# Optimization experiments

Measured on AMD Instinct MI355X. Metric: run time of the kernel, lower is better.

## Reference

```python
import jax, jax.numpy as jnp
import numpy as np

B, S, D, H = 4, 2048, 1024, 16
DK = D // H  # 64


def setup_inputs() -> dict:
    key = jax.random.key(0)
    ks = jax.random.split(key, 5)
    scale = 1.0 / np.sqrt(D)
    return {
        "embeddings": jax.random.normal(ks[0], (B, S, D), dtype=jnp.float32),
        "W_q": jax.random.normal(ks[1], (D, D), dtype=jnp.float32) * scale,
        "W_k": jax.random.normal(ks[2], (D, D), dtype=jnp.float32) * scale,
        "W_v": jax.random.normal(ks[3], (D, D), dtype=jnp.float32) * scale,
        "W_o": jax.random.normal(ks[4], (D, D), dtype=jnp.float32) * scale,
    }


def reference(embeddings, W_q, W_k, W_v, W_o):
    # torch nn.Linear: y = x @ W.T  (weights are [out, in])
    b, s, d = embeddings.shape
    h, dk = H, DK
    q = embeddings @ W_q.T  # [b, s, d]
    k = embeddings @ W_k.T
    v = embeddings @ W_v.T
    # split heads along last dim (matches the per-head slicing in the torch loop)
    q = q.reshape(b, s, h, dk)
    k = k.reshape(b, s, h, dk)
    v = v.reshape(b, s, h, dk)
    scores = jnp.einsum("bqhd,bkhd->bhqk", q, k) / jnp.sqrt(jnp.float32(dk))
    p = jax.nn.softmax(scores, axis=-1)  # dropout is identity at eval
    ctx = jnp.einsum("bhqk,bkhd->bqhd", p, v).reshape(b, s, d)
    return ctx @ W_o.T
```

## Files before the change

### kernel.cpp

```cpp
#include <hip/hip_runtime.h>
#include <hip/hip_bf16.h>

typedef unsigned short u16;
typedef __attribute__((ext_vector_type(8))) short bf16x8;
typedef __attribute__((ext_vector_type(4))) float f32x4;

#define AS1 __attribute__((address_space(1)))
#define AS3 __attribute__((address_space(3)))

constexpr int Bc = 4, Sc = 2048, Dc = 1024, Hc = 16, DKc = 64;
constexpr size_t EDc = (size_t)Bc * Sc * Dc;
constexpr size_t WDc = (size_t)Dc * Dc;

__device__ __forceinline__ void g2l16(const void* g, void* l) {
  __builtin_amdgcn_global_load_lds((const AS1 unsigned int*)g,
                                   (AS3 unsigned int*)l, 16, 0, 0);
}

__device__ __forceinline__ u16 f2b(float f) {
  union { float f; unsigned u; } x; x.f = f;
  unsigned r = x.u + 0x7fffu + ((x.u >> 16) & 1u);
  return (u16)(r >> 16);
}

#if __has_builtin(__builtin_amdgcn_cvt_pk_bf16_f32)
typedef __attribute__((ext_vector_type(2))) __bf16 hbf2;
__device__ __forceinline__ unsigned f2b_pk(float a, float b) {
  union { hbf2 v; unsigned u; } x;
  x.v = __builtin_amdgcn_cvt_pk_bf16_f32(a, b);
  return x.u;
}
#else
__device__ __forceinline__ unsigned f2b_pk(float a, float b) {
  return (unsigned)f2b(a) | ((unsigned)f2b(b) << 16);
}
#endif

__device__ __forceinline__ float fast_exp2(float x) {
#if __has_builtin(__builtin_amdgcn_exp2f)
  return __builtin_amdgcn_exp2f(x);
#else
  return exp2f(x);
#endif
}

__global__ __launch_bounds__(256)
void cvt_all(const float* __restrict__ e, const float* __restrict__ wq,
             const float* __restrict__ wk, const float* __restrict__ wv,
             const float* __restrict__ wo, u16* __restrict__ dst) {
  int bx = blockIdx.x;
  const float* src;
  size_t doff;
  int chunk;
  if (bx < 4096) {
    src = e; doff = 0; chunk = bx;
  } else {
    int t = bx - 4096;
    int w = t >> 9;
    chunk = t & 511;
    src = (w == 0) ? wq : (w == 1) ? wk : (w == 2) ? wv : wo;
    doff = EDc + (size_t)w * WDc;
  }
  size_t i = ((size_t)chunk * 256 + threadIdx.x) * 8;
  float4 a = *(const float4*)(src + i);
  float4 b = *(const float4*)(src + i + 4);
  bf16x8 o;
  o[0] = (short)f2b(a.x); o[1] = (short)f2b(a.y);
  o[2] = (short)f2b(a.z); o[3] = (short)f2b(a.w);
  o[4] = (short)f2b(b.x); o[5] = (short)f2b(b.y);
  o[6] = (short)f2b(b.z); o[7] = (short)f2b(b.w);
  *(bf16x8*)(dst + doff + i) = o;
}

__global__ __launch_bounds__(256, 2)
void gemm_qkv(const u16* __restrict__ X, const u16* __restrict__ Wq,
              const u16* __restrict__ Wk, const u16* __restrict__ Wv,
              u16* __restrict__ Qo, u16* __restrict__ Ko,
              u16* __restrict__ VTo) {
  constexpr int BM = 128, BK = 64, K = Dc, N = Dc;
  __shared__ u16 As[BM * BK];
  __shared__ u16 Bs[BM * BK];

  const int tid = threadIdx.x;
  const int wave = tid >> 6, lane = tid & 63;
  const int mr = lane & 15, quad = lane >> 4, mr7 = lane & 7;
  const int hwlin = blockIdx.y * 24 + blockIdx.x;
  const int swz = (hwlin & 7) * 192 + (hwlin >> 3);
  const int lx = swz % 24, ly = swz / 24;
  const int sect = lx >> 3;
  const int n0 = (lx & 7) * 128;
  const int m0 = ly * BM;
  const u16* W = (sect == 0) ? Wq : (sect == 1) ? Wk : Wv;
  const int wm = (wave >> 1) * 64, wn = (wave & 1) * 64;
  const int ldr = lane >> 3;
  const int ldc_sw = ((lane & 7) ^ (ldr & 7)) * 8;
  const bool vsec = (sect == 2);

  const f32x4 zero = {0.f, 0.f, 0.f, 0.f};
  f32x4 acc[4][4];
  #pragma unroll
  for (int i = 0; i < 4; i++)
    #pragma unroll
    for (int j = 0; j < 4; j++) acc[i][j] = zero;

  for (int k0 = 0; k0 < K; k0 += BK) {
    __syncthreads();
    #pragma unroll
    for (int i = 0; i < 4; i++) {
      int row = wave * 32 + i * 8;
      g2l16(X + (size_t)(m0 + row + ldr) * K + k0 + ldc_sw, As + row * BK);
      g2l16(W + (size_t)(n0 + row + ldr) * K + k0 + ldc_sw, Bs + row * BK);
    }
    __syncthreads();

    #pragma unroll
    for (int c = 0; c < 2; c++) {
      bf16x8 a[4], b[4];
      #pragma unroll
      for (int i = 0; i < 4; i++)
        a[i] = *(const bf16x8*)(As + (wm + i * 16 + mr) * BK +
                                (((c * 4 + quad) ^ mr7) * 8));
      #pragma unroll
      for (int j = 0; j < 4; j++)
        b[j] = *(const bf16x8*)(Bs + (wn + j * 16 + mr) * BK +
                                (((c * 4 + quad) ^ mr7) * 8));
      if (vsec) {
        #pragma unroll
        for (int i = 0; i < 4; i++)
          #pragma unroll
          for (int j = 0; j < 4; j++)
            acc[i][j] = __builtin_amdgcn_mfma_f32_16x16x32_bf16(
                b[j], a[i], acc[i][j], 0, 0, 0);
      } else {
        #pragma unroll
        for (int i = 0; i < 4; i++)
          #pragma unroll
          for (int j = 0; j < 4; j++)
            acc[i][j] = __builtin_amdgcn_mfma_f32_16x16x32_bf16(
                a[i], b[j], acc[i][j], 0, 0, 0);
      }
    }
  }

  if (vsec) {
    #pragma unroll
    for (int i = 0; i < 4; i++) {
      int s_glob = m0 + wm + i * 16 + mr;
      int bb = s_glob >> 11, s = s_glob & 2047;
      int sp = (s & ~63) | (s & 32) | ((s & 12) << 1) | ((s & 16) >> 2) |
               (s & 3);
      #pragma unroll
      for (int j = 0; j < 4; j++) {
        int nbase = n0 + wn + j * 16 + quad * 4;
        #pragma unroll
        for (int r = 0; r < 4; r++) {
          int n = nbase + r;
          int h = n >> 6, d = n & 63;
          VTo[((size_t)((bb * Hc + h) * DKc + d)) * Sc + sp] = f2b(acc[i][j][r]);
        }
      }
    }
  } else {
    const float scale = (sect == 0) ? 0.18033688f : 1.0f;
    u16* Y = (sect == 0) ? Qo : Ko;
    #pragma unroll
    for (int i = 0; i < 4; i++)
      #pragma unroll
      for (int j = 0; j < 4; j++)
        #pragma unroll
        for (int r = 0; r < 4; r++) {
          int m = m0 + wm + i * 16 + quad * 4 + r;
          int n = n0 + wn + j * 16 + mr;
          Y[(size_t)m * N + n] = f2b(acc[i][j][r] * scale);
        }
  }
}

__global__ __launch_bounds__(256, 2)
void gemm_out(const u16* __restrict__ X, const u16* __restrict__ W,
              float* __restrict__ Y, int M, int N, int K) {
  constexpr int BM = 128, BK = 64;
  __shared__ u16 As[BM * BK];
  __shared__ u16 Bs[BM * BK];

  const int tid = threadIdx.x;
  const int wave = tid >> 6, lane = tid & 63;
  const int mr = lane & 15, quad = lane >> 4, mr7 = lane & 7;
  const int hwlin = blockIdx.y * 8 + blockIdx.x;
  const int swz = (hwlin & 7) * 64 + (hwlin >> 3);
  const int m0 = (swz >> 3) * BM, n0 = (swz & 7) * BM;
  const int wm = (wave >> 1) * 64, wn = (wave & 1) * 64;
  const int ldr = lane >> 3;
  const int ldc_sw = ((lane & 7) ^ (ldr & 7)) * 8;

  const f32x4 zero = {0.f, 0.f, 0.f, 0.f};
  f32x4 acc[4][4];
  #pragma unroll
  for (int i = 0; i < 4; i++)
    #pragma unroll
    for (int j = 0; j < 4; j++) acc[i][j] = zero;

  for (int k0 = 0; k0 < K; k0 += BK) {
    __syncthreads();
    #pragma unroll
    for (int i = 0; i < 4; i++) {
      int row = wave * 32 + i * 8;
      g2l16(X + (size_t)(m0 + row + ldr) * K + k0 + ldc_sw, As + row * BK);
      g2l16(W + (size_t)(n0 + row + ldr) * K + k0 + ldc_sw, Bs + row * BK);
    }
    __syncthreads();

    #pragma unroll
    for (int c = 0; c < 2; c++) {
      bf16x8 a[4], b[4];
      #pragma unroll
      for (int i = 0; i < 4; i++)
        a[i] = *(const bf16x8*)(As + (wm + i * 16 + mr) * BK +
                                (((c * 4 + quad) ^ mr7) * 8));
      #pragma unroll
      for (int j = 0; j < 4; j++)
        b[j] = *(const bf16x8*)(Bs + (wn + j * 16 + mr) * BK +
                                (((c * 4 + quad) ^ mr7) * 8));
      #pragma unroll
      for (int i = 0; i < 4; i++)
        #pragma unroll
        for (int j = 0; j < 4; j++)
          acc[i][j] = __builtin_amdgcn_mfma_f32_16x16x32_bf16(
              a[i], b[j], acc[i][j], 0, 0, 0);
    }
  }

  #pragma unroll
  for (int i = 0; i < 4; i++)
    #pragma unroll
    for (int j = 0; j < 4; j++)
      #pragma unroll
      for (int r = 0; r < 4; r++) {
        int m = m0 + wm + i * 16 + quad * 4 + r;
        int n = n0 + wn + j * 16 + mr;
        Y[(size_t)m * N + n] = acc[i][j][r];
      }
}

__global__ __launch_bounds__(512, 4)
void attn(const u16* __restrict__ Q, const u16* __restrict__ K,
          const u16* __restrict__ VT, u16* __restrict__ O) {
  __shared__ u16 Ks[2][64 * 64];
  __shared__ u16 Vs[2][64 * 64];

  const int tid = threadIdx.x;
  const int wave = tid >> 6, lane = tid & 63;
  const int mr = lane & 15, quad = lane >> 4, mr7 = lane & 7;
  const int hwlin = blockIdx.y * 8 + blockIdx.x;
  const int swz = (hwlin & 7) * 64 + (hwlin >> 3);
  const int bh = swz >> 3;
  const int q0 = (swz & 7) * 256;
  const int b = bh >> 4, h = bh & 15;
  const size_t headK = (size_t)b * Sc * Dc + (size_t)h * DKc;
  const size_t headV = (size_t)bh * DKc * Sc;
  const int ldr = lane >> 3;
  const int ldc_sw = ((lane & 7) ^ (ldr & 7)) * 8;

  const int row0 = wave * 8;
  const int pr = row0 + ldr;

  bf16x8 qa[2][2];
  #pragma unroll
  for (int sub = 0; sub < 2; sub++)
    #pragma unroll
    for (int c = 0; c < 2; c++)
      qa[sub][c] = *(const bf16x8*)(Q + headK +
          (size_t)(q0 + wave * 32 + sub * 16 + mr) * Dc + c * 32 + quad * 8);

  const f32x4 zero = {0.f, 0.f, 0.f, 0.f};
  const short one_bf = (short)0x3F80;
  const bf16x8 ones = {one_bf, one_bf, one_bf, one_bf,
                       one_bf, one_bf, one_bf, one_bf};
  f32x4 o[2][4];
  f32x4 lacc[2];
  #pragma unroll
  for (int sub = 0; sub < 2; sub++) {
    lacc[sub] = zero;
    #pragma unroll
    for (int i = 0; i < 4; i++) o[sub][i] = zero;
  }

  g2l16(K + headK + (size_t)pr * Dc + ldc_sw, Ks[0] + row0 * 64);
  g2l16(VT + headV + (size_t)pr * Sc + ldc_sw, Vs[0] + row0 * 64);
  __syncthreads();

  union W8 { unsigned u[4]; bf16x8 v; };

  for (int kt = 0; kt < Sc / 64; kt++) {
    const int cur = kt & 1;
    if (kt + 1 < Sc / 64) {
      const int nk0 = (kt + 1) * 64;
      const int nxt = cur ^ 1;
      g2l16(K + headK + (size_t)(nk0 + pr) * Dc + ldc_sw, Ks[nxt] + row0 * 64);
      g2l16(VT + headV + (size_t)pr * Sc + nk0 + ldc_sw, Vs[nxt] + row0 * 64);
    }

    f32x4 s0[4], s1[4];
    #pragma unroll
    for (int kc = 0; kc < 4; kc++) {
      bf16x8 k0 = *(const bf16x8*)(Ks[cur] + (kc * 16 + mr) * 64 +
                                   ((quad ^ mr7) * 8));
      bf16x8 k1 = *(const bf16x8*)(Ks[cur] + (kc * 16 + mr) * 64 +
                                   (((4 + quad) ^ mr7) * 8));
      __builtin_amdgcn_s_setprio(1);
      s0[kc] = __builtin_amdgcn_mfma_f32_16x16x32_bf16(k0, qa[0][0], zero, 0, 0, 0);
      s1[kc] = __builtin_amdgcn_mfma_f32_16x16x32_bf16(k0, qa[1][0], zero, 0, 0, 0);
      s0[kc] = __builtin_amdgcn_mfma_f32_16x16x32_bf16(k1, qa[0][1], s0[kc], 0, 0, 0);
      s1[kc] = __builtin_amdgcn_mfma_f32_16x16x32_bf16(k1, qa[1][1], s1[kc], 0, 0, 0);
      __builtin_amdgcn_s_setprio(0);
    }

    W8 paw[2][2];
    {
      float e[16];
      #pragma unroll
      for (int kc = 0; kc < 4; kc++)
        #pragma unroll
        for (int r = 0; r < 4; r++)
          e[kc * 4 + r] = fast_exp2(s0[kc][r]);
      paw[0][0].u[0] = f2b_pk(e[0], e[1]);
      paw[0][0].u[1] = f2b_pk(e[2], e[3]);
      paw[0][0].u[2] = f2b_pk(e[4], e[5]);
      paw[0][0].u[3] = f2b_pk(e[6], e[7]);
      paw[0][1].u[0] = f2b_pk(e[8], e[9]);
      paw[0][1].u[1] = f2b_pk(e[10], e[11]);
      paw[0][1].u[2] = f2b_pk(e[12], e[13]);
      paw[0][1].u[3] = f2b_pk(e[14], e[15]);
    }
    {
      float e[16];
      #pragma unroll
      for (int kc = 0; kc < 4; kc++)
        #pragma unroll
        for (int r = 0; r < 4; r++)
          e[kc * 4 + r] = fast_exp2(s1[kc][r]);
      paw[1][0].u[0] = f2b_pk(e[0], e[1]);
      paw[1][0].u[1] = f2b_pk(e[2], e[3]);
      paw[1][0].u[2] = f2b_pk(e[4], e[5]);
      paw[1][0].u[3] = f2b_pk(e[6], e[7]);
      paw[1][1].u[0] = f2b_pk(e[8], e[9]);
      paw[1][1].u[1] = f2b_pk(e[10], e[11]);
      paw[1][1].u[2] = f2b_pk(e[12], e[13]);
      paw[1][1].u[3] = f2b_pk(e[14], e[15]);
    }

    __builtin_amdgcn_s_setprio(1);
    lacc[0] = __builtin_amdgcn_mfma_f32_16x16x32_bf16(
        paw[0][0].v, ones, lacc[0], 0, 0, 0);
    lacc[0] = __builtin_amdgcn_mfma_f32_16x16x32_bf16(
        paw[0][1].v, ones, lacc[0], 0, 0, 0);
    lacc[1] = __builtin_amdgcn_mfma_f32_16x16x32_bf16(
        paw[1][0].v, ones, lacc[1], 0, 0, 0);
    lacc[1] = __builtin_amdgcn_mfma_f32_16x16x32_bf16(
        paw[1][1].v, ones, lacc[1], 0, 0, 0);
    __builtin_amdgcn_s_setprio(0);

    #pragma unroll
    for (int ni = 0; ni < 4; ni++) {
      bf16x8 v0 = *(const bf16x8*)(Vs[cur] + (ni * 16 + mr) * 64 +
                                   ((quad ^ mr7) * 8));
      bf16x8 v1 = *(const bf16x8*)(Vs[cur] + (ni * 16 + mr) * 64 +
                                   (((4 + quad) ^ mr7) * 8));
      __builtin_amdgcn_s_setprio(1);
      o[0][ni] = __builtin_amdgcn_mfma_f32_16x16x32_bf16(
          paw[0][0].v, v0, o[0][ni], 0, 0, 0);
      o[1][ni] = __builtin_amdgcn_mfma_f32_16x16x32_bf16(
          paw[1][0].v, v0, o[1][ni], 0, 0, 0);
      o[0][ni] = __builtin_amdgcn_mfma_f32_16x16x32_bf16(
          paw[0][1].v, v1, o[0][ni], 0, 0, 0);
      o[1][ni] = __builtin_amdgcn_mfma_f32_16x16x32_bf16(
          paw[1][1].v, v1, o[1][ni], 0, 0, 0);
      __builtin_amdgcn_s_setprio(0);
    }

    __syncthreads();
  }

  #pragma unroll
  for (int sub = 0; sub < 2; sub++) {
    #pragma unroll
    for (int r = 0; r < 4; r++) {
      float inv = 1.0f / lacc[sub][r];
      int qq = q0 + wave * 32 + sub * 16 + quad * 4 + r;
      #pragma unroll
      for (int ni = 0; ni < 4; ni++)
        O[headK + (size_t)qq * Dc + ni * 16 + mr] = f2b(o[sub][ni][r] * inv);
    }
  }
}

extern "C" void kernel_launch(void* const* d_in, const int* in_sizes, int n_in,
                              void* d_out, int out_size, void* d_ws, size_t ws_size,
                              hipStream_t stream) {
  const float* emb = (const float*)d_in[0];
  const float* Wq  = (const float*)d_in[1];
  const float* Wk  = (const float*)d_in[2];
  const float* Wv  = (const float*)d_in[3];
  const float* Wo  = (const float*)d_in[4];
  float* out = (float*)d_out;

  const int M = Bc * Sc;

  u16* Eb  = (u16*)d_ws;
  u16* Wqb = Eb  + EDc;
  u16* Wkb = Wqb + WDc;
  u16* Wvb = Wkb + WDc;
  u16* Wob = Wvb + WDc;
  u16* Qb  = Wob + WDc;
  u16* Kb  = Qb  + EDc;
  u16* VTb = Kb  + EDc;
  u16* Cb  = Qb;

  dim3 blk(256);
  cvt_all<<<dim3(4096 + 4 * 512), blk, 0, stream>>>(emb, Wq, Wk, Wv, Wo, Eb);

  gemm_qkv<<<dim3(24, M / 128), blk, 0, stream>>>(Eb, Wqb, Wkb, Wvb,
                                                  Qb, Kb, VTb);

  attn<<<dim3(Sc / 256, Bc * Hc), dim3(512), 0, stream>>>(Qb, Kb, VTb, Cb);

  gemm_out<<<dim3(Dc / 128, M / 128), blk, 0, stream>>>(Cb, Wob, out,
                                                        M, Dc, Dc);
}
```

Before: 257.5 us.

## Software-pipeline attention: overlap QK^T of tile k with PV of tile k-1

Restructures the attention inner loop so each iteration computes scores and exponentials for the current KV tile while doing the row-sum and PV MFMAs for the previous tile's probabilities. V gets a triple-buffered LDS slot so the previous tile's values stay resident while the next one is prefetched. The loop is unrolled by two with ping-pong probability registers, and a drain step after the loop handles the last tile. The aim is to let exp/convert VALU work overlap with MFMA work, at the cost of more registers and LDS that could reduce occupancy.

```diff
diff --git a/kernel.cpp b/kernel.cpp
--- a/kernel.cpp
+++ b/kernel.cpp
@@ -246,7 +246,7 @@
 void attn(const u16* __restrict__ Q, const u16* __restrict__ K,
           const u16* __restrict__ VT, u16* __restrict__ O) {
   __shared__ u16 Ks[2][64 * 64];
-  __shared__ u16 Vs[2][64 * 64];
+  __shared__ u16 Vs[3][64 * 64];
 
   const int tid = threadIdx.x;
   const int wave = tid >> 6, lane = tid & 63;
@@ -285,101 +285,121 @@
     for (int i = 0; i < 4; i++) o[sub][i] = zero;
   }
 
+  union W8 { unsigned u[4]; bf16x8 v; };
+  W8 pawA[2][2], pawB[2][2];
+  #pragma unroll
+  for (int sb = 0; sb < 2; sb++)
+    #pragma unroll
+    for (int hh = 0; hh < 2; hh++) {
+      pawA[sb][hh].u[0] = 0; pawA[sb][hh].u[1] = 0;
+      pawA[sb][hh].u[2] = 0; pawA[sb][hh].u[3] = 0;
+    }
+
   g2l16(K + headK + (size_t)pr * Dc + ldc_sw, Ks[0] + row0 * 64);
   g2l16(VT + headV + (size_t)pr * Sc + ldc_sw, Vs[0] + row0 * 64);
   __syncthreads();
 
-  union W8 { unsigned u[4]; bf16x8 v; };
-
-  for (int kt = 0; kt < Sc / 64; kt++) {
-    const int cur = kt & 1;
+  int c0 = 0, cprev = 0;
+
+  auto body = [&](int kt, W8 (&pprev)[2][2], W8 (&pnew)[2][2]) {
+    const int curK = kt & 1;
+    const int cw = (c0 == 2) ? 0 : c0 + 1;
+    const int cp = cprev;
     if (kt + 1 < Sc / 64) {
       const int nk0 = (kt + 1) * 64;
-      const int nxt = cur ^ 1;
-      g2l16(K + headK + (size_t)(nk0 + pr) * Dc + ldc_sw, Ks[nxt] + row0 * 64);
-      g2l16(VT + headV + (size_t)pr * Sc + nk0 + ldc_sw, Vs[nxt] + row0 * 64);
-    }
-
-    f32x4 s0[4], s1[4];
-    #pragma unroll
-    for (int kc = 0; kc < 4; kc++) {
-      bf16x8 k0 = *(const bf16x8*)(Ks[cur] + (kc * 16 + mr) * 64 +
-                                   ((quad ^ mr7) * 8));
-      bf16x8 k1 = *(const bf16x8*)(Ks[cur] + (kc * 16 + mr) * 64 +
-                                   (((4 + quad) ^ mr7) * 8));
+      g2l16(K + headK + (size_t)(nk0 + pr) * Dc + ldc_sw,
+            Ks[curK ^ 1] + row0 * 64);
+      g2l16(VT + headV + (size_t)pr * Sc + nk0 + ldc_sw,
+            Vs[cw] + row0 * 64);
+    }
+
+    #pragma unroll
+    for (int sub = 0; sub < 2; sub++) {
+      f32x4 s[4];
       __builtin_amdgcn_s_setprio(1);
-      s0[kc] = __builtin_amdgcn_mfma_f32_16x16x32_bf16(k0, qa[0][0], zero, 0, 0, 0);
-      s1[kc] = __builtin_amdgcn_mfma_f32_16x16x32_bf16(k0, qa[1][0], zero, 0, 0, 0);
-      s0[kc] = __builtin_amdgcn_mfma_f32_16x16x32_bf16(k1, qa[0][1], s0[kc], 0, 0, 0);
-      s1[kc] = __builtin_amdgcn_mfma_f32_16x16x32_bf16(k1, qa[1][1], s1[kc], 0, 0, 0);
+      #pragma unroll
+      for (int kc = 0; kc < 4; kc++) {
+        bf16x8 k0 = *(const bf16x8*)(Ks[curK] + (kc * 16 + mr) * 64 +
+                                     ((quad ^ mr7) * 8));
+        bf16x8 k1 = *(const bf16x8*)(Ks[curK] + (kc * 16 + mr) * 64 +
+                                     (((4 + quad) ^ mr7) * 8));
+        s[kc] = __builtin_amdgcn_mfma_f32_16x16x32_bf16(
+            k0, qa[sub][0], zero, 0, 0, 0);
+        s[kc] = __builtin_amdgcn_mfma_f32_16x16x32_bf16(
+            k1, qa[sub][1], s[kc], 0, 0, 0);
+      }
       __builtin_amdgcn_s_setprio(0);
-    }
-
-    W8 paw[2][2];
-    {
-      float e[16];
-      #pragma unroll
-      for (int kc = 0; kc < 4; kc++)
-        #pragma unroll
-        for (int r = 0; r < 4; r++)
-          e[kc * 4 + r] = fast_exp2(s0[kc][r]);
-      paw[0][0].u[0] = f2b_pk(e[0], e[1]);
-      paw[0][0].u[1] = f2b_pk(e[2], e[3]);
-      paw[0][0].u[2] = f2b_pk(e[4], e[5]);
-      paw[0][0].u[3] = f2b_pk(e[6], e[7]);
-      paw[0][1].u[0] = f2b_pk(e[8], e[9]);
-      paw[0][1].u[1] = f2b_pk(e[10], e[11]);
-      paw[0][1].u[2] = f2b_pk(e[12], e[13]);
-      paw[0][1].u[3] = f2b_pk(e[14], e[15]);
-    }
-    {
-      float e[16];
-      #pragma unroll
-      for (int kc = 0; kc < 4; kc++)
-        #pragma unroll
-        for (int r = 0; r < 4; r++)
-          e[kc * 4 + r] = fast_exp2(s1[kc][r]);
-      paw[1][0].u[0] = f2b_pk(e[0], e[1]);
-      paw[1][0].u[1] = f2b_pk(e[2], e[3]);
-      paw[1][0].u[2] = f2b_pk(e[4], e[5]);
-      paw[1][0].u[3] = f2b_pk(e[6], e[7]);
-      paw[1][1].u[0] = f2b_pk(e[8], e[9]);
-      paw[1][1].u[1] = f2b_pk(e[10], e[11]);
-      paw[1][1].u[2] = f2b_pk(e[12], e[13]);
-      paw[1][1].u[3] = f2b_pk(e[14], e[15]);
+      pnew[sub][0].u[0] = f2b_pk(fast_exp2(s[0][0]), fast_exp2(s[0][1]));
+      pnew[sub][0].u[1] = f2b_pk(fast_exp2(s[0][2]), fast_exp2(s[0][3]));
+      pnew[sub][0].u[2] = f2b_pk(fast_exp2(s[1][0]), fast_exp2(s[1][1]));
+      pnew[sub][0].u[3] = f2b_pk(fast_exp2(s[1][2]), fast_exp2(s[1][3]));
+      pnew[sub][1].u[0] = f2b_pk(fast_exp2(s[2][0]), fast_exp2(s[2][1]));
+      pnew[sub][1].u[1] = f2b_pk(fast_exp2(s[2][2]), fast_exp2(s[2][3]));
+      pnew[sub][1].u[2] = f2b_pk(fast_exp2(s[3][0]), fast_exp2(s[3][1]));
+      pnew[sub][1].u[3] = f2b_pk(fast_exp2(s[3][2]), fast_exp2(s[3][3]));
     }
 
     __builtin_amdgcn_s_setprio(1);
     lacc[0] = __builtin_amdgcn_mfma_f32_16x16x32_bf16(
-        paw[0][0].v, ones, lacc[0], 0, 0, 0);
+        pprev[0][0].v, ones, lacc[0], 0, 0, 0);
     lacc[0] = __builtin_amdgcn_mfma_f32_16x16x32_bf16(
-        paw[0][1].v, ones, lacc[0], 0, 0, 0);
+        pprev[0][1].v, ones, lacc[0], 0, 0, 0);
     lacc[1] = __builtin_amdgcn_mfma_f32_16x16x32_bf16(
-        paw[1][0].v, ones, lacc[1], 0, 0, 0);
+        pprev[1][0].v, ones, lacc[1], 0, 0, 0);
     lacc[1] = __builtin_amdgcn_mfma_f32_16x16x32_bf16(
-        paw[1][1].v, ones, lacc[1], 0, 0, 0);
+        pprev[1][1].v, ones, lacc[1], 0, 0, 0);
+    #pragma unroll
+    for (int ni = 0; ni < 4; ni++) {
+      bf16x8 v0 = *(const bf16x8*)(Vs[cp] + (ni * 16 + mr) * 64 +
+                                   ((quad ^ mr7) * 8));
+      bf16x8 v1 = *(const bf16x8*)(Vs[cp] + (ni * 16 + mr) * 64 +
+                                   (((4 + quad) ^ mr7) * 8));
+      o[0][ni] = __builtin_amdgcn_mfma_f32_16x16x32_bf16(
+          pprev[0][0].v, v0, o[0][ni], 0, 0, 0);
+      o[1][ni] = __builtin_amdgcn_mfma_f32_16x16x32_bf16(
+          pprev[1][0].v, v0, o[1][ni], 0, 0, 0);
+      o[0][ni] = __builtin_amdgcn_mfma_f32_16x16x32_bf16(
+          pprev[0][1].v, v1, o[0][ni], 0, 0, 0);
+      o[1][ni] = __builtin_amdgcn_mfma_f32_16x16x32_bf16(
+          pprev[1][1].v, v1, o[1][ni], 0, 0, 0);
+    }
     __builtin_amdgcn_s_setprio(0);
 
-    #pragma unroll
-    for (int ni = 0; ni < 4; ni++) {
-      bf16x8 v0 = *(const bf16x8*)(Vs[cur] + (ni * 16 + mr) * 64 +
-                                   ((quad ^ mr7) * 8));
-      bf16x8 v1 = *(const bf16x8*)(Vs[cur] + (ni * 16 + mr) * 64 +
-                                   (((4 + quad) ^ mr7) * 8));
-      __builtin_amdgcn_s_setprio(1);
-      o[0][ni] = __builtin_amdgcn_mfma_f32_16x16x32_bf16(
-          paw[0][0].v, v0, o[0][ni], 0, 0, 0);
-      o[1][ni] = __builtin_amdgcn_mfma_f32_16x16x32_bf16(
-          paw[1][0].v, v0, o[1][ni], 0, 0, 0);
-      o[0][ni] = __builtin_amdgcn_mfma_f32_16x16x32_bf16(
-          paw[0][1].v, v1, o[0][ni], 0, 0, 0);
-      o[1][ni] = __builtin_amdgcn_mfma_f32_16x16x32_bf16(
-          paw[1][1].v, v1, o[1][ni], 0, 0, 0);
-      __builtin_amdgcn_s_setprio(0);
-    }
-
     __syncthreads();
-  }
+    cprev = c0;
+    c0 = cw;
+  };
+
+  for (int kt = 0; kt < Sc / 64; kt += 2) {
+    body(kt, pawA, pawB);
+    body(kt + 1, pawB, pawA);
+  }
+
+  __builtin_amdgcn_s_setprio(1);
+  lacc[0] = __builtin_amdgcn_mfma_f32_16x16x32_bf16(
+      pawA[0][0].v, ones, lacc[0], 0, 0, 0);
+  lacc[0] = __builtin_amdgcn_mfma_f32_16x16x32_bf16(
+      pawA[0][1].v, ones, lacc[0], 0, 0, 0);
+  lacc[1] = __builtin_amdgcn_mfma_f32_16x16x32_bf16(
+      pawA[1][0].v, ones, lacc[1], 0, 0, 0);
+  lacc[1] = __builtin_amdgcn_mfma_f32_16x16x32_bf16(
+      pawA[1][1].v, ones, lacc[1], 0, 0, 0);
+  #pragma unroll
+  for (int ni = 0; ni < 4; ni++) {
+    bf16x8 v0 = *(const bf16x8*)(Vs[cprev] + (ni * 16 + mr) * 64 +
+                                 ((quad ^ mr7) * 8));
+    bf16x8 v1 = *(const bf16x8*)(Vs[cprev] + (ni * 16 + mr) * 64 +
+                                 (((4 + quad) ^ mr7) * 8));
+    o[0][ni] = __builtin_amdgcn_mfma_f32_16x16x32_bf16(
+        pawA[0][0].v, v0, o[0][ni], 0, 0, 0);
+    o[1][ni] = __builtin_amdgcn_mfma_f32_16x16x32_bf16(
+        pawA[1][0].v, v0, o[1][ni], 0, 0, 0);
+    o[0][ni] = __builtin_amdgcn_mfma_f32_16x16x32_bf16(
+        pawA[0][1].v, v1, o[0][ni], 0, 0, 0);
+    o[1][ni] = __builtin_amdgcn_mfma_f32_16x16x32_bf16(
+        pawA[1][1].v, v1, o[1][ni], 0, 0, 0);
+  }
+  __builtin_amdgcn_s_setprio(0);
 
   #pragma unroll
   for (int sub = 0; sub < 2; sub++) {
```

Result: slower. 265.5 us (+3.1%).

## Halve attention query tile to 128 rows, doubling grid size

Applied to the files above, without the earlier changes.

Each attention block now handles 128 query rows (16 per wave) instead of 256 (32 per wave), and the grid doubles to 1024 blocks with the block-index swizzle adjusted to match. This cuts registers per thread and gives more blocks for filling CUs and hiding latency. In exchange, each K/V tile loaded into LDS is reused by half as many queries, so total K/V global traffic and LDS reads per unit of MFMA work double. The priority-raise region also now spans the PV MFMA loop as a whole.

```diff
diff --git a/kernel.cpp b/kernel.cpp
--- a/kernel.cpp
+++ b/kernel.cpp
@@ -251,10 +251,10 @@
   const int tid = threadIdx.x;
   const int wave = tid >> 6, lane = tid & 63;
   const int mr = lane & 15, quad = lane >> 4, mr7 = lane & 7;
-  const int hwlin = blockIdx.y * 8 + blockIdx.x;
-  const int swz = (hwlin & 7) * 64 + (hwlin >> 3);
-  const int bh = swz >> 3;
-  const int q0 = (swz & 7) * 256;
+  const int hwlin = blockIdx.y * 16 + blockIdx.x;
+  const int swz = (hwlin & 7) * 128 + (hwlin >> 3);
+  const int bh = swz >> 4;
+  const int q0 = (swz & 15) * 128;
   const int b = bh >> 4, h = bh & 15;
   const size_t headK = (size_t)b * Sc * Dc + (size_t)h * DKc;
   const size_t headV = (size_t)bh * DKc * Sc;
@@ -264,26 +264,20 @@
   const int row0 = wave * 8;
   const int pr = row0 + ldr;
 
-  bf16x8 qa[2][2];
-  #pragma unroll
-  for (int sub = 0; sub < 2; sub++)
-    #pragma unroll
-    for (int c = 0; c < 2; c++)
-      qa[sub][c] = *(const bf16x8*)(Q + headK +
-          (size_t)(q0 + wave * 32 + sub * 16 + mr) * Dc + c * 32 + quad * 8);
+  bf16x8 qa[2];
+  #pragma unroll
+  for (int c = 0; c < 2; c++)
+    qa[c] = *(const bf16x8*)(Q + headK +
+        (size_t)(q0 + wave * 16 + mr) * Dc + c * 32 + quad * 8);
 
   const f32x4 zero = {0.f, 0.f, 0.f, 0.f};
   const short one_bf = (short)0x3F80;
   const bf16x8 ones = {one_bf, one_bf, one_bf, one_bf,
                        one_bf, one_bf, one_bf, one_bf};
-  f32x4 o[2][4];
-  f32x4 lacc[2];
-  #pragma unroll
-  for (int sub = 0; sub < 2; sub++) {
-    lacc[sub] = zero;
-    #pragma unroll
-    for (int i = 0; i < 4; i++) o[sub][i] = zero;
-  }
+  f32x4 o[4];
+  f32x4 lacc = zero;
+  #pragma unroll
+  for (int i = 0; i < 4; i++) o[i] = zero;
 
   g2l16(K + headK + (size_t)pr * Dc + ldc_sw, Ks[0] + row0 * 64);
   g2l16(VT + headV + (size_t)pr * Sc + ldc_sw, Vs[0] + row0 * 64);
@@ -300,7 +294,7 @@
       g2l16(VT + headV + (size_t)pr * Sc + nk0 + ldc_sw, Vs[nxt] + row0 * 64);
     }
 
-    f32x4 s0[4], s1[4];
+    f32x4 s[4];
     #pragma unroll
     for (int kc = 0; kc < 4; kc++) {
       bf16x8 k0 = *(const bf16x8*)(Ks[cur] + (kc * 16 + mr) * 64 +
@@ -308,57 +302,24 @@
       bf16x8 k1 = *(const bf16x8*)(Ks[cur] + (kc * 16 + mr) * 64 +
                                    (((4 + quad) ^ mr7) * 8));
       __builtin_amdgcn_s_setprio(1);
-      s0[kc] = __builtin_amdgcn_mfma_f32_16x16x32_bf16(k0, qa[0][0], zero, 0, 0, 0);
-      s1[kc] = __builtin_amdgcn_mfma_f32_16x16x32_bf16(k0, qa[1][0], zero, 0, 0, 0);
-      s0[kc] = __builtin_amdgcn_mfma_f32_16x16x32_bf16(k1, qa[0][1], s0[kc], 0, 0, 0);
-      s1[kc] = __builtin_amdgcn_mfma_f32_16x16x32_bf16(k1, qa[1][1], s1[kc], 0, 0, 0);
+      s[kc] = __builtin_amdgcn_mfma_f32_16x16x32_bf16(k0, qa[0], zero, 0, 0, 0);
+      s[kc] = __builtin_amdgcn_mfma_f32_16x16x32_bf16(k1, qa[1], s[kc], 0, 0, 0);
       __builtin_amdgcn_s_setprio(0);
     }
 
-    W8 paw[2][2];
-    {
-      float e[16];
-      #pragma unroll
-      for (int kc = 0; kc < 4; kc++)
-        #pragma unroll
-        for (int r = 0; r < 4; r++)
-          e[kc * 4 + r] = fast_exp2(s0[kc][r]);
-      paw[0][0].u[0] = f2b_pk(e[0], e[1]);
-      paw[0][0].u[1] = f2b_pk(e[2], e[3]);
-      paw[0][0].u[2] = f2b_pk(e[4], e[5]);
-      paw[0][0].u[3] = f2b_pk(e[6], e[7]);
-      paw[0][1].u[0] = f2b_pk(e[8], e[9]);
-      paw[0][1].u[1] = f2b_pk(e[10], e[11]);
-      paw[0][1].u[2] = f2b_pk(e[12], e[13]);
-      paw[0][1].u[3] = f2b_pk(e[14], e[15]);
-    }
-    {
-      float e[16];
-      #pragma unroll
-      for (int kc = 0; kc < 4; kc++)
-        #pragma unroll
-        for (int r = 0; r < 4; r++)
-          e[kc * 4 + r] = fast_exp2(s1[kc][r]);
-      paw[1][0].u[0] = f2b_pk(e[0], e[1]);
-      paw[1][0].u[1] = f2b_pk(e[2], e[3]);
-      paw[1][0].u[2] = f2b_pk(e[4], e[5]);
-      paw[1][0].u[3] = f2b_pk(e[6], e[7]);
-      paw[1][1].u[0] = f2b_pk(e[8], e[9]);
-      paw[1][1].u[1] = f2b_pk(e[10], e[11]);
-      paw[1][1].u[2] = f2b_pk(e[12], e[13]);
-      paw[1][1].u[3] = f2b_pk(e[14], e[15]);
-    }
+    W8 paw0, paw1;
+    paw0.u[0] = f2b_pk(fast_exp2(s[0][0]), fast_exp2(s[0][1]));
+    paw0.u[1] = f2b_pk(fast_exp2(s[0][2]), fast_exp2(s[0][3]));
+    paw0.u[2] = f2b_pk(fast_exp2(s[1][0]), fast_exp2(s[1][1]));
+    paw0.u[3] = f2b_pk(fast_exp2(s[1][2]), fast_exp2(s[1][3]));
+    paw1.u[0] = f2b_pk(fast_exp2(s[2][0]), fast_exp2(s[2][1]));
+    paw1.u[1] = f2b_pk(fast_exp2(s[2][2]), fast_exp2(s[2][3]));
+    paw1.u[2] = f2b_pk(fast_exp2(s[3][0]), fast_exp2(s[3][1]));
+    paw1.u[3] = f2b_pk(fast_exp2(s[3][2]), fast_exp2(s[3][3]));
 
     __builtin_amdgcn_s_setprio(1);
-    lacc[0] = __builtin_amdgcn_mfma_f32_16x16x32_bf16(
-        paw[0][0].v, ones, lacc[0], 0, 0, 0);
-    lacc[0] = __builtin_amdgcn_mfma_f32_16x16x32_bf16(
-        paw[0][1].v, ones, lacc[0], 0, 0, 0);
-    lacc[1] = __builtin_amdgcn_mfma_f32_16x16x32_bf16(
-        paw[1][0].v, ones, lacc[1], 0, 0, 0);
-    lacc[1] = __builtin_amdgcn_mfma_f32_16x16x32_bf16(
-        paw[1][1].v, ones, lacc[1], 0, 0, 0);
-    __builtin_amdgcn_s_setprio(0);
+    lacc = __builtin_amdgcn_mfma_f32_16x16x32_bf16(paw0.v, ones, lacc, 0, 0, 0);
+    lacc = __builtin_amdgcn_mfma_f32_16x16x32_bf16(paw1.v, ones, lacc, 0, 0, 0);
 
     #pragma unroll
     for (int ni = 0; ni < 4; ni++) {
@@ -366,31 +327,21 @@
                                    ((quad ^ mr7) * 8));
       bf16x8 v1 = *(const bf16x8*)(Vs[cur] + (ni * 16 + mr) * 64 +
                                    (((4 + quad) ^ mr7) * 8));
-      __builtin_amdgcn_s_setprio(1);
-      o[0][ni] = __builtin_amdgcn_mfma_f32_16x16x32_bf16(
-          paw[0][0].v, v0, o[0][ni], 0, 0, 0);
-      o[1][ni] = __builtin_amdgcn_mfma_f32_16x16x32_bf16(
-          paw[1][0].v, v0, o[1][ni], 0, 0, 0);
-      o[0][ni] = __builtin_amdgcn_mfma_f32_16x16x32_bf16(
-          paw[0][1].v, v1, o[0][ni], 0, 0, 0);
-      o[1][ni] = __builtin_amdgcn_mfma_f32_16x16x32_bf16(
-          paw[1][1].v, v1, o[1][ni], 0, 0, 0);
-      __builtin_amdgcn_s_setprio(0);
-    }
-
-    __syncthreads();
-  }
-
-  #pragma unroll
-  for (int sub = 0; sub < 2; sub++) {
-    #pragma unroll
-    for (int r = 0; r < 4; r++) {
-      float inv = 1.0f / lacc[sub][r];
-      int qq = q0 + wave * 32 + sub * 16 + quad * 4 + r;
-      #pragma unroll
-      for (int ni = 0; ni < 4; ni++)
-        O[headK + (size_t)qq * Dc + ni * 16 + mr] = f2b(o[sub][ni][r] * inv);
-    }
+      o[ni] = __builtin_amdgcn_mfma_f32_16x16x32_bf16(paw0.v, v0, o[ni], 0, 0, 0);
+      o[ni] = __builtin_amdgcn_mfma_f32_16x16x32_bf16(paw1.v, v1, o[ni], 0, 0, 0);
+    }
+    __builtin_amdgcn_s_setprio(0);
+
+    __syncthreads();
+  }
+
+  #pragma unroll
+  for (int r = 0; r < 4; r++) {
+    float inv = 1.0f / lacc[r];
+    int qq = q0 + wave * 16 + quad * 4 + r;
+    #pragma unroll
+    for (int ni = 0; ni < 4; ni++)
+      O[headK + (size_t)qq * Dc + ni * 16 + mr] = f2b(o[ni][r] * inv);
   }
 }
 
@@ -422,7 +373,7 @@
   gemm_qkv<<<dim3(24, M / 128), blk, 0, stream>>>(Eb, Wqb, Wkb, Wvb,
                                                   Qb, Kb, VTb);
 
-  attn<<<dim3(Sc / 256, Bc * Hc), dim3(512), 0, stream>>>(Qb, Kb, VTb, Cb);
+  attn<<<dim3(Sc / 128, Bc * Hc), dim3(512), 0, stream>>>(Qb, Kb, VTb, Cb);
 
   gemm_out<<<dim3(Dc / 128, M / 128), blk, 0, stream>>>(Cb, Wob, out,
                                                         M, Dc, Dc);
```

New measurement: 260.0 us. Within noise of the previous version (+1.0%).
